# Kernel optimization log

Measured on AMD Instinct MI355X. Metric: run time of the kernel, lower is better.

## Reference

```python
import jax, jax.numpy as jnp
import numpy as np

D_MODEL = 1024
N_HEADS = 16
D_K = D_MODEL // N_HEADS


def setup_inputs() -> dict:
    key = jax.random.key(0)
    ks = jax.random.split(key, 12)
    B, S, D, H = 2, 2048, D_MODEL, N_HEADS
    s = 1.0 / np.sqrt(D)
    inp = {
        "x": jax.random.normal(ks[0], (B, S, D), jnp.float32),
        "Wq": jax.random.normal(ks[1], (D, D), jnp.float32) * s,
        "bq": jnp.zeros((D,), jnp.float32),
        "Wk": jax.random.normal(ks[2], (D, D), jnp.float32) * s,
        "bk": jnp.zeros((D,), jnp.float32),
        "Wv": jax.random.normal(ks[3], (D, D), jnp.float32) * s,
        "bv": jnp.zeros((D,), jnp.float32),
        "Wo": jax.random.normal(ks[4], (D, D), jnp.float32) * s,
        "bo": jnp.zeros((D,), jnp.float32),
        "Wp": jax.random.normal(ks[5], (D, H), jnp.float32) * s,
        "bp": jnp.zeros((H,), jnp.float32),
        "alpha": jax.random.normal(ks[6], (H,), jnp.float32) * 0.1,
    }
    return inp


def reference(x, Wq, bq, Wk, bk, Wv, bv, Wo, bo, Wp, bp, alpha):
    B, S, D = x.shape
    H, dk = N_HEADS, D_K
    scale = dk ** -0.5
    # projections -> (B, H, S, dk)
    Q = (x @ Wq + bq).reshape(B, S, H, dk).transpose(0, 2, 1, 3)
    K = (x @ Wk + bk).reshape(B, S, H, dk).transpose(0, 2, 1, 3)
    V = (x @ Wv + bv).reshape(B, S, H, dk).transpose(0, 2, 1, 3)
    scores = jnp.einsum("bhid,bhjd->bhij", Q, K) * scale  # (B,H,S,S)
    # phase derived from x: (B,S,H) -> (B,H,S)
    phase = (x @ Wp + bp).transpose(0, 2, 1)
    # coherence(i,j) = cos(phi_i - phi_j), per batch/head
    coherence = jnp.cos(phase[:, :, :, None] - phase[:, :, None, :])
    scores = scores + alpha[None, :, None, None] * coherence
    attn = jax.nn.softmax(scores, axis=-1)
    out = jnp.einsum("bhij,bhjd->bhid", attn, V)  # (B,H,S,dk)
    out = out.transpose(0, 2, 1, 3).reshape(B, S, D)
    return out @ Wo + bo
```

## Files before the change

kernel.cpp:

```cpp
#include <hip/hip_runtime.h>
#include <math.h>


#define S_LEN 2048
#define NHEADS 16

typedef __attribute__((ext_vector_type(8))) short short8;
typedef __attribute__((ext_vector_type(4))) float floatx4;
typedef __attribute__((ext_vector_type(2))) float float2v;
typedef __attribute__((ext_vector_type(4))) unsigned int uintx4;

__device__ inline unsigned short f2bf(float f) {
    union { float f; unsigned int i; } v; v.f = f;
    unsigned int u = v.i;
    return (unsigned short)((u + 0x7fffu + ((u >> 16) & 1u)) >> 16);
}
__device__ inline unsigned int pack2_bf16(float hi, float lo) {
    union { float f; unsigned int u; } a, b; a.f = hi; b.f = lo;
    return __builtin_amdgcn_perm(a.u, b.u, 0x07060302u);
}
__device__ inline void async_copy16(const unsigned short* src, unsigned short* dst_lds) {
    __builtin_amdgcn_global_load_lds(
        (const __attribute__((address_space(1))) unsigned int*)(src),
        (__attribute__((address_space(3))) unsigned int*)(dst_lds), 16, 0, 0);
}
__device__ inline void async_copy4(const float* src, float* dst_lds) {
    __builtin_amdgcn_global_load_lds(
        (const __attribute__((address_space(1))) unsigned int*)(src),
        (__attribute__((address_space(3))) unsigned int*)(dst_lds), 4, 0, 0);
}

__global__ __launch_bounds__(256) void prep_kernel(
    const float* __restrict__ x, const float* __restrict__ Wp,
    const float* __restrict__ bp,
    const float* __restrict__ w0, const float* __restrict__ w1,
    const float* __restrict__ w2, const float* __restrict__ w3,
    unsigned short* __restrict__ d0, unsigned short* __restrict__ d1,
    unsigned short* __restrict__ d2, unsigned short* __restrict__ d3,
    float* __restrict__ cosP, float* __restrict__ sinP,
    unsigned short* __restrict__ xb) {
    __shared__ __align__(16) unsigned short shmem[64 * 72];
    int t = threadIdx.x;
    if (blockIdx.x < 4096) {
        float* red = reinterpret_cast<float*>(shmem);
        int bid = blockIdx.x;
        int b = bid >> 11, s = bid & 2047;
        int h = t & 15, c = t >> 4;
        const float* xr = x + (size_t)bid * 1024;
        {
            float4 xv = *reinterpret_cast<const float4*>(&xr[t * 4]);
            uint2 o;
            o.x = (unsigned int)f2bf(xv.x) | ((unsigned int)f2bf(xv.y) << 16);
            o.y = (unsigned int)f2bf(xv.z) | ((unsigned int)f2bf(xv.w) << 16);
            *reinterpret_cast<uint2*>(&xb[(size_t)bid * 1024 + t * 4]) = o;
        }
        float acc = 0.f;
#pragma unroll 8
        for (int kk = 0; kk < 64; kk++) {
            int k = c * 64 + kk;
            acc += xr[k] * Wp[k * 16 + h];
        }
        red[t] = acc;
        __syncthreads();
        if (t < 16) {
            float sum = 0.f;
#pragma unroll
            for (int c2 = 0; c2 < 16; c2++) sum += red[c2 * 16 + t];
            sum += bp[t];
            float sv, cv;
            __sincosf(sum, &sv, &cv);
            size_t o = ((size_t)b * NHEADS + t) * S_LEN + s;
            cosP[o] = cv; sinP[o] = sv;
        }
    } else {
        unsigned short (*tile)[72] = reinterpret_cast<unsigned short (*)[72]>(shmem);
        int bid = blockIdx.x - 4096;
        int mat = bid >> 8;
        int tl  = bid & 255;
        int tr = tl >> 4, tc = tl & 15;
        const float* src    = (mat == 0) ? w0 : (mat == 1) ? w1 : (mat == 2) ? w2 : w3;
        unsigned short* dst = (mat == 0) ? d0 : (mat == 1) ? d1 : (mat == 2) ? d2 : d3;
        int col = t & 63, rbase = (t >> 6) * 16;
#pragma unroll
        for (int i = 0; i < 16; i++) {
            int row = rbase + i;
            tile[row][col] = f2bf(src[(size_t)(tr * 64 + row) * 1024 + tc * 64 + col]);
        }
        __syncthreads();
#pragma unroll
        for (int i = 0; i < 16; i++) {
            int row = rbase + i;
            dst[(size_t)(tc * 64 + row) * 1024 + tr * 64 + col] = tile[col][row];
        }
    }
}

template <int MT>
__global__ __launch_bounds__(256) void gemm_bt(
    const unsigned short* __restrict__ A, const unsigned short* __restrict__ BT,
    int N, int mode,
    const float* __restrict__ b0, const float* __restrict__ b1,
    const float* __restrict__ b2,
    unsigned short* __restrict__ o0, unsigned short* __restrict__ o1,
    unsigned short* __restrict__ o2, float* __restrict__ of) {
    __shared__ __align__(16) unsigned short As[MT * 32];
    __shared__ __align__(16) unsigned short Bs[128 * 32];
    const int K = 1024;
    const int MI = MT / 32;
    int t = threadIdx.x;
    int mBase = blockIdx.x * MT;
    int nBase = blockIdx.y * 128;
    int w = t >> 6, lane = t & 63, l15 = lane & 15, quad = lane >> 4;
    int wm = (w & 1) * (MT / 2), wn = (w >> 1) * 64;
    floatx4 acc[MI][4];
#pragma unroll
    for (int i = 0; i < MI; i++)
#pragma unroll
        for (int j = 0; j < 4; j++) acc[i][j] = (floatx4){0.f, 0.f, 0.f, 0.f};

    int arow = t >> 2, aseg = (t & 3) * 8;
    for (int k0 = 0; k0 < K; k0 += 32) {
        __syncthreads();
#pragma unroll
        for (int i = 0; i < MT / 64; i++)
            async_copy16(&A[(size_t)(mBase + i * 64 + arow) * K + k0 + aseg],
                         &As[(i * 64 + arow) * 32 + aseg]);
#pragma unroll
        for (int i = 0; i < 2; i++)
            async_copy16(&BT[(size_t)(nBase + i * 64 + arow) * K + k0 + aseg],
                         &Bs[(i * 64 + arow) * 32 + aseg]);
        __syncthreads();
        short8 af[MI], bfr[4];
#pragma unroll
        for (int mi = 0; mi < MI; mi++)
            af[mi] = *reinterpret_cast<const short8*>(&As[(wm + mi * 16 + l15) * 32 + quad * 8]);
#pragma unroll
        for (int ni = 0; ni < 4; ni++)
            bfr[ni] = *reinterpret_cast<const short8*>(&Bs[(wn + ni * 16 + l15) * 32 + quad * 8]);
#pragma unroll
        for (int mi = 0; mi < MI; mi++)
#pragma unroll
            for (int ni = 0; ni < 4; ni++)
                acc[mi][ni] = __builtin_amdgcn_mfma_f32_16x16x32_bf16(af[mi], bfr[ni], acc[mi][ni], 0, 0, 0);
    }

#pragma unroll
    for (int mi = 0; mi < MI; mi++) {
        int rowB = mBase + wm + mi * 16 + quad * 4;
#pragma unroll
        for (int ni = 0; ni < 4; ni++) {
            int col = nBase + wn + ni * 16 + l15;
            if (mode == 0) {
                float bias = b0[col];
#pragma unroll
                for (int r = 0; r < 4; r++) {
                    of[(size_t)(rowB + r) * N + col] = acc[mi][ni][r] + bias;
                }
            } else {
                int mat = col >> 10, nn = col & 1023;
                int h = nn >> 6, d = nn & 63;
                int b = rowB >> 11, sidx = rowB & 2047;
                if (mat == 2) {
                    float bv = b2[nn];
                    int jj = sidx & 63;
                    int a2 = jj >> 5, c2 = (jj >> 4) & 1, bb = jj & 15;
                    size_t rowOff = ((size_t)((b * NHEADS + h) * 64 + d)) * S_LEN +
                                    (sidx & ~63) + a2 * 32 + c2;
#pragma unroll
                    for (int r = 0; r < 4; r++)
                        o2[rowOff + 2 * (bb + r)] = f2bf(acc[mi][ni][r] + bv);
                } else {
                    const float* bias  = (mat == 0) ? b0 : b1;
                    unsigned short* op = (mat == 0) ? o0 : o1;
                    float bv = bias[nn];
                    float scl = (mat == 0) ? 0.18033688f : 1.0f;
#pragma unroll
                    for (int r = 0; r < 4; r++) {
                        float cv = (acc[mi][ni][r] + bv) * scl;
                        op[(((size_t)b * NHEADS + h) * S_LEN + (sidx + r)) * 64 + d] = f2bf(cv);
                    }
                }
            }
        }
    }
}

__global__ __launch_bounds__(1024) void attn_kernel(
    const unsigned short* __restrict__ Qg, const unsigned short* __restrict__ Kg,
    const unsigned short* __restrict__ VTg,
    const float* __restrict__ cosP, const float* __restrict__ sinP,
    const float* __restrict__ alpha, unsigned short* __restrict__ ctx) {
    __shared__ __align__(16) unsigned short KsB[2][64 * 64];
    __shared__ __align__(16) unsigned short VtB[2][64 * 64];
    __shared__ __align__(16) float csB[2][128];
    __shared__ __align__(16) unsigned short Plb[16][16 * 72];

    int x = blockIdx.x;
    int bh = (x & 7) * 4 + (x >> 6);
    int qt = (x >> 3) & 7;
    int t = threadIdx.x, w = t >> 6, lane = t & 63, l15 = lane & 15, quad = lane >> 4;
    int m0 = qt * 256 + w * 16;
    size_t base = (size_t)bh * (S_LEN * 64);
    size_t phBase = (size_t)bh * S_LEN;
    const float L2E = 1.44269504f;

    int th = t & 511;
    int sj = th >> 3, sg = th & 7;
    int srot = ((sg - (sj & 7)) & 7) * 8;
    bool stK = (t < 512);

    short8 qf[2];
#pragma unroll
    for (int c = 0; c < 2; c++)
        qf[c] = *reinterpret_cast<const short8*>(
            &Qg[base + (size_t)(m0 + l15) * 64 + c * 32 + quad * 8]);

    float alph = alpha[bh & 15] * L2E;
    float2v ci2[2], si2[2];
#pragma unroll
    for (int hh = 0; hh < 2; hh++) {
        size_t o = phBase + m0 + quad * 4 + hh * 2;
        ci2[hh] = (float2v){alph * cosP[o], alph * cosP[o + 1]};
        si2[hh] = (float2v){alph * sinP[o], alph * sinP[o + 1]};
    }

    {
        if (stK) async_copy16(&Kg[base + (size_t)sj * 64 + srot], &KsB[0][th * 8]);
        else     async_copy16(&VTg[base + (size_t)sj * S_LEN + srot], &VtB[0][th * 8]);
        if (w == 4)      async_copy4(&cosP[phBase + lane], &csB[0][lane]);
        else if (w == 5) async_copy4(&sinP[phBase + lane], &csB[0][64 + lane]);
    }

    floatx4 oacc[4], lacc;
#pragma unroll
    for (int tt = 0; tt < 4; tt++) oacc[tt] = (floatx4){0.f, 0.f, 0.f, 0.f};
    lacc = (floatx4){0.f, 0.f, 0.f, 0.f};
    const short8 ones8 = {(short)0x3F80, (short)0x3F80, (short)0x3F80, (short)0x3F80,
                          (short)0x3F80, (short)0x3F80, (short)0x3F80, (short)0x3F80};

    int rot = l15 & 7;
    int cb0 = 16 * ((quad + rot) & 7);
    int cb1 = 16 * ((quad + 4 + rot) & 7);

    for (int kt = 0; kt < 32; kt++) {
        int p = kt & 1;
        __syncthreads();
        if (kt < 31) {
            int kn = kt + 1, pn = p ^ 1;
            if (stK) async_copy16(&Kg[base + (size_t)(kn * 64 + sj) * 64 + srot], &KsB[pn][th * 8]);
            else     async_copy16(&VTg[base + (size_t)sj * S_LEN + kn * 64 + srot], &VtB[pn][th * 8]);
            if (w == 4)      async_copy4(&cosP[phBase + kn * 64 + lane], &csB[pn][lane]);
            else if (w == 5) async_copy4(&sinP[phBase + kn * 64 + lane], &csB[pn][64 + lane]);
        }

        floatx4 st[4];
#pragma unroll
        for (int jt = 0; jt < 4; jt++) {
            const char* kr = (const char*)&KsB[p][(jt * 16 + l15) * 64];
            short8 kf0 = *reinterpret_cast<const short8*>(kr + cb0);
            short8 kf1 = *reinterpret_cast<const short8*>(kr + cb1);
            floatx4 s = (floatx4){0.f, 0.f, 0.f, 0.f};
            s = __builtin_amdgcn_mfma_f32_16x16x32_bf16(qf[0], kf0, s, 0, 0, 0);
            s = __builtin_amdgcn_mfma_f32_16x16x32_bf16(qf[1], kf1, s, 0, 0, 0);
            st[jt] = s;
        }

        float cjv[4], sjv[4];
#pragma unroll
        for (int jt = 0; jt < 4; jt++) {
            cjv[jt] = csB[p][jt * 16 + l15];
            sjv[jt] = csB[p][64 + jt * 16 + l15];
        }

        unsigned int* pl = reinterpret_cast<unsigned int*>(&Plb[w][0]);
#pragma unroll
        for (int rp = 0; rp < 2; rp++) {
            float2v a0, a1, a2, a3;
            {
                float2v s0 = (float2v){st[0][rp * 2], st[0][rp * 2 + 1]};
                float2v s1 = (float2v){st[1][rp * 2], st[1][rp * 2 + 1]};
                float2v s2 = (float2v){st[2][rp * 2], st[2][rp * 2 + 1]};
                float2v s3 = (float2v){st[3][rp * 2], st[3][rp * 2 + 1]};
                a0 = si2[rp] * sjv[0] + (ci2[rp] * cjv[0] + s0);
                a1 = si2[rp] * sjv[1] + (ci2[rp] * cjv[1] + s1);
                a2 = si2[rp] * sjv[2] + (ci2[rp] * cjv[2] + s2);
                a3 = si2[rp] * sjv[3] + (ci2[rp] * cjv[3] + s3);
            }
            int row = quad * 4 + rp * 2;
            pl[row * 36 + l15]      = pack2_bf16(__builtin_amdgcn_exp2f(a1.x),
                                                 __builtin_amdgcn_exp2f(a0.x));
            pl[row * 36 + 16 + l15] = pack2_bf16(__builtin_amdgcn_exp2f(a3.x),
                                                 __builtin_amdgcn_exp2f(a2.x));
            pl[(row + 1) * 36 + l15]      = pack2_bf16(__builtin_amdgcn_exp2f(a1.y),
                                                       __builtin_amdgcn_exp2f(a0.y));
            pl[(row + 1) * 36 + 16 + l15] = pack2_bf16(__builtin_amdgcn_exp2f(a3.y),
                                                       __builtin_amdgcn_exp2f(a2.y));
        }

        short8 pf[2];
#pragma unroll
        for (int c = 0; c < 2; c++)
            pf[c] = *reinterpret_cast<const short8*>(
                &Plb[w][l15 * 72 + c * 32 + quad * 8]);

#pragma unroll
        for (int c = 0; c < 2; c++) {
            int cb = c ? cb1 : cb0;
#pragma unroll
            for (int tt = 0; tt < 4; tt++) {
                const char* vr = (const char*)&VtB[p][(tt * 16 + l15) * 64];
                short8 vf = *reinterpret_cast<const short8*>(vr + cb);
                oacc[tt] = __builtin_amdgcn_mfma_f32_16x16x32_bf16(pf[c], vf, oacc[tt], 0, 0, 0);
            }
            lacc = __builtin_amdgcn_mfma_f32_16x16x32_bf16(pf[c], ones8, lacc, 0, 0, 0);
        }
    }

    int b = bh >> 4, h = bh & 15;
    float inv[4];
#pragma unroll
    for (int r = 0; r < 4; r++) inv[r] = 1.0f / lacc[r];
#pragma unroll
    for (int tt = 0; tt < 4; tt++)
#pragma unroll
        for (int r = 0; r < 4; r++) {
            int srow = m0 + quad * 4 + r;
            ctx[((size_t)(b * S_LEN + srow)) * 1024 + h * 64 + tt * 16 + l15] =
                f2bf(oacc[tt][r] * inv[r]);
        }
}

extern "C" void kernel_launch(void* const* d_in, const int* in_sizes, int n_in,
                              void* d_out, int out_size, void* d_ws, size_t ws_size,
                              hipStream_t stream) {
    const float* x     = (const float*)d_in[0];
    const float* Wq    = (const float*)d_in[1];
    const float* bq    = (const float*)d_in[2];
    const float* Wk    = (const float*)d_in[3];
    const float* bk    = (const float*)d_in[4];
    const float* Wv    = (const float*)d_in[5];
    const float* bv    = (const float*)d_in[6];
    const float* Wo    = (const float*)d_in[7];
    const float* bo    = (const float*)d_in[8];
    const float* Wp    = (const float*)d_in[9];
    const float* bp    = (const float*)d_in[10];
    const float* alpha = (const float*)d_in[11];
    float* out = (float*)d_out;

    const size_t MB = 1048576;
    char* ws = (char*)d_ws;
    unsigned short* WT   = (unsigned short*)(ws);
    unsigned short* WoT  = (unsigned short*)(ws + 6 * MB);
    unsigned short* xb   = (unsigned short*)(ws + 8 * MB);
    unsigned short* ctx  = (unsigned short*)(ws + 8 * MB);
    unsigned short* Qw   = (unsigned short*)(ws + 16 * MB);
    unsigned short* Kw   = (unsigned short*)(ws + 24 * MB);
    unsigned short* VTg  = (unsigned short*)(ws + 32 * MB);
    float* cosP          = (float*)(ws + 40 * MB);
    float* sinP          = (float*)(ws + 40 * MB + 262144);

    prep_kernel<<<dim3(5120), dim3(256), 0, stream>>>(
        x, Wp, bp, Wq, Wk, Wv, Wo,
        WT, WT + 1048576, WT + 2097152, WoT, cosP, sinP, xb);
    gemm_bt<128><<<dim3(32, 24), dim3(256), 0, stream>>>(
        xb, WT, 3072, 1, bq, bk, bv, Qw, Kw, VTg, (float*)nullptr);
    attn_kernel<<<dim3(256), dim3(1024), 0, stream>>>(
        Qw, Kw, VTg, cosP, sinP, alpha, ctx);
    gemm_bt<64><<<dim3(64, 8), dim3(256), 0, stream>>>(
        ctx, WoT, 1024, 0, bo, bo, bo,
        (unsigned short*)nullptr, (unsigned short*)nullptr,
        (unsigned short*)nullptr, out);
}
```

Before: 215.2 us.

## Give each attention wave two 16-row query tiles with half the threads per block

The attention kernel now launches 512 threads per block instead of 1024, and each wave handles 32 query rows as two 16-row sub-tiles. K/V fragments loaded from LDS are reused across both sub-tiles, which halves LDS reads per score and PV MFMA. Each thread now issues both the K and the V async copy. The change doubles accumulator and Q register state per wave, which raises register pressure, and it halves the waves per block available to hide latency.

```diff
diff --git a/kernel.cpp b/kernel.cpp
--- a/kernel.cpp
+++ b/kernel.cpp
@@ -185,7 +185,7 @@
     }
 }
 
-__global__ __launch_bounds__(1024) void attn_kernel(
+__global__ __launch_bounds__(512, 4) void attn_kernel(
     const unsigned short* __restrict__ Qg, const unsigned short* __restrict__ Kg,
     const unsigned short* __restrict__ VTg,
     const float* __restrict__ cosP, const float* __restrict__ sinP,
@@ -193,48 +193,53 @@
     __shared__ __align__(16) unsigned short KsB[2][64 * 64];
     __shared__ __align__(16) unsigned short VtB[2][64 * 64];
     __shared__ __align__(16) float csB[2][128];
-    __shared__ __align__(16) unsigned short Plb[16][16 * 72];
+    __shared__ __align__(16) unsigned short Plb[8][32 * 72];
 
     int x = blockIdx.x;
     int bh = (x & 7) * 4 + (x >> 6);
     int qt = (x >> 3) & 7;
     int t = threadIdx.x, w = t >> 6, lane = t & 63, l15 = lane & 15, quad = lane >> 4;
-    int m0 = qt * 256 + w * 16;
+    int m0 = qt * 256 + w * 32;
     size_t base = (size_t)bh * (S_LEN * 64);
     size_t phBase = (size_t)bh * S_LEN;
     const float L2E = 1.44269504f;
 
-    int th = t & 511;
-    int sj = th >> 3, sg = th & 7;
+    int sj = t >> 3, sg = t & 7;
     int srot = ((sg - (sj & 7)) & 7) * 8;
-    bool stK = (t < 512);
-
-    short8 qf[2];
-#pragma unroll
-    for (int c = 0; c < 2; c++)
-        qf[c] = *reinterpret_cast<const short8*>(
-            &Qg[base + (size_t)(m0 + l15) * 64 + c * 32 + quad * 8]);
+
+    short8 qf[2][2];
+#pragma unroll
+    for (int rh = 0; rh < 2; rh++)
+#pragma unroll
+        for (int c = 0; c < 2; c++)
+            qf[rh][c] = *reinterpret_cast<const short8*>(
+                &Qg[base + (size_t)(m0 + rh * 16 + l15) * 64 + c * 32 + quad * 8]);
 
     float alph = alpha[bh & 15] * L2E;
-    float2v ci2[2], si2[2];
-#pragma unroll
-    for (int hh = 0; hh < 2; hh++) {
-        size_t o = phBase + m0 + quad * 4 + hh * 2;
-        ci2[hh] = (float2v){alph * cosP[o], alph * cosP[o + 1]};
-        si2[hh] = (float2v){alph * sinP[o], alph * sinP[o + 1]};
-    }
+    float2v ci2[2][2], si2[2][2];
+#pragma unroll
+    for (int rh = 0; rh < 2; rh++)
+#pragma unroll
+        for (int hh = 0; hh < 2; hh++) {
+            size_t o = phBase + m0 + rh * 16 + quad * 4 + hh * 2;
+            ci2[rh][hh] = (float2v){alph * cosP[o], alph * cosP[o + 1]};
+            si2[rh][hh] = (float2v){alph * sinP[o], alph * sinP[o + 1]};
+        }
 
     {
-        if (stK) async_copy16(&Kg[base + (size_t)sj * 64 + srot], &KsB[0][th * 8]);
-        else     async_copy16(&VTg[base + (size_t)sj * S_LEN + srot], &VtB[0][th * 8]);
-        if (w == 4)      async_copy4(&cosP[phBase + lane], &csB[0][lane]);
-        else if (w == 5) async_copy4(&sinP[phBase + lane], &csB[0][64 + lane]);
-    }
-
-    floatx4 oacc[4], lacc;
-#pragma unroll
-    for (int tt = 0; tt < 4; tt++) oacc[tt] = (floatx4){0.f, 0.f, 0.f, 0.f};
-    lacc = (floatx4){0.f, 0.f, 0.f, 0.f};
+        async_copy16(&Kg[base + (size_t)sj * 64 + srot], &KsB[0][t * 8]);
+        async_copy16(&VTg[base + (size_t)sj * S_LEN + srot], &VtB[0][t * 8]);
+        if (w == 2)      async_copy4(&cosP[phBase + lane], &csB[0][lane]);
+        else if (w == 3) async_copy4(&sinP[phBase + lane], &csB[0][64 + lane]);
+    }
+
+    floatx4 oacc[2][4], lacc[2];
+#pragma unroll
+    for (int rh = 0; rh < 2; rh++) {
+#pragma unroll
+        for (int tt = 0; tt < 4; tt++) oacc[rh][tt] = (floatx4){0.f, 0.f, 0.f, 0.f};
+        lacc[rh] = (floatx4){0.f, 0.f, 0.f, 0.f};
+    }
     const short8 ones8 = {(short)0x3F80, (short)0x3F80, (short)0x3F80, (short)0x3F80,
                           (short)0x3F80, (short)0x3F80, (short)0x3F80, (short)0x3F80};
 
@@ -247,22 +252,25 @@
         __syncthreads();
         if (kt < 31) {
             int kn = kt + 1, pn = p ^ 1;
-            if (stK) async_copy16(&Kg[base + (size_t)(kn * 64 + sj) * 64 + srot], &KsB[pn][th * 8]);
-            else     async_copy16(&VTg[base + (size_t)sj * S_LEN + kn * 64 + srot], &VtB[pn][th * 8]);
-            if (w == 4)      async_copy4(&cosP[phBase + kn * 64 + lane], &csB[pn][lane]);
-            else if (w == 5) async_copy4(&sinP[phBase + kn * 64 + lane], &csB[pn][64 + lane]);
-        }
-
-        floatx4 st[4];
+            async_copy16(&Kg[base + (size_t)(kn * 64 + sj) * 64 + srot], &KsB[pn][t * 8]);
+            async_copy16(&VTg[base + (size_t)sj * S_LEN + kn * 64 + srot], &VtB[pn][t * 8]);
+            if (w == 2)      async_copy4(&cosP[phBase + kn * 64 + lane], &csB[pn][lane]);
+            else if (w == 3) async_copy4(&sinP[phBase + kn * 64 + lane], &csB[pn][64 + lane]);
+        }
+
+        floatx4 st[2][4];
 #pragma unroll
         for (int jt = 0; jt < 4; jt++) {
             const char* kr = (const char*)&KsB[p][(jt * 16 + l15) * 64];
             short8 kf0 = *reinterpret_cast<const short8*>(kr + cb0);
             short8 kf1 = *reinterpret_cast<const short8*>(kr + cb1);
-            floatx4 s = (floatx4){0.f, 0.f, 0.f, 0.f};
-            s = __builtin_amdgcn_mfma_f32_16x16x32_bf16(qf[0], kf0, s, 0, 0, 0);
-            s = __builtin_amdgcn_mfma_f32_16x16x32_bf16(qf[1], kf1, s, 0, 0, 0);
-            st[jt] = s;
+#pragma unroll
+            for (int rh = 0; rh < 2; rh++) {
+                floatx4 s = (floatx4){0.f, 0.f, 0.f, 0.f};
+                s = __builtin_amdgcn_mfma_f32_16x16x32_bf16(qf[rh][0], kf0, s, 0, 0, 0);
+                s = __builtin_amdgcn_mfma_f32_16x16x32_bf16(qf[rh][1], kf1, s, 0, 0, 0);
+                st[rh][jt] = s;
+            }
         }
 
         float cjv[4], sjv[4];
@@ -274,34 +282,38 @@
 
         unsigned int* pl = reinterpret_cast<unsigned int*>(&Plb[w][0]);
 #pragma unroll
-        for (int rp = 0; rp < 2; rp++) {
-            float2v a0, a1, a2, a3;
-            {
-                float2v s0 = (float2v){st[0][rp * 2], st[0][rp * 2 + 1]};
-                float2v s1 = (float2v){st[1][rp * 2], st[1][rp * 2 + 1]};
-                float2v s2 = (float2v){st[2][rp * 2], st[2][rp * 2 + 1]};
-                float2v s3 = (float2v){st[3][rp * 2], st[3][rp * 2 + 1]};
-                a0 = si2[rp] * sjv[0] + (ci2[rp] * cjv[0] + s0);
-                a1 = si2[rp] * sjv[1] + (ci2[rp] * cjv[1] + s1);
-                a2 = si2[rp] * sjv[2] + (ci2[rp] * cjv[2] + s2);
-                a3 = si2[rp] * sjv[3] + (ci2[rp] * cjv[3] + s3);
-            }
-            int row = quad * 4 + rp * 2;
-            pl[row * 36 + l15]      = pack2_bf16(__builtin_amdgcn_exp2f(a1.x),
-                                                 __builtin_amdgcn_exp2f(a0.x));
-            pl[row * 36 + 16 + l15] = pack2_bf16(__builtin_amdgcn_exp2f(a3.x),
-                                                 __builtin_amdgcn_exp2f(a2.x));
-            pl[(row + 1) * 36 + l15]      = pack2_bf16(__builtin_amdgcn_exp2f(a1.y),
-                                                       __builtin_amdgcn_exp2f(a0.y));
-            pl[(row + 1) * 36 + 16 + l15] = pack2_bf16(__builtin_amdgcn_exp2f(a3.y),
-                                                       __builtin_amdgcn_exp2f(a2.y));
-        }
-
-        short8 pf[2];
-#pragma unroll
-        for (int c = 0; c < 2; c++)
-            pf[c] = *reinterpret_cast<const short8*>(
-                &Plb[w][l15 * 72 + c * 32 + quad * 8]);
+        for (int rh = 0; rh < 2; rh++)
+#pragma unroll
+            for (int rp = 0; rp < 2; rp++) {
+                float2v a0, a1, a2, a3;
+                {
+                    float2v s0 = (float2v){st[rh][0][rp * 2], st[rh][0][rp * 2 + 1]};
+                    float2v s1 = (float2v){st[rh][1][rp * 2], st[rh][1][rp * 2 + 1]};
+                    float2v s2 = (float2v){st[rh][2][rp * 2], st[rh][2][rp * 2 + 1]};
+                    float2v s3 = (float2v){st[rh][3][rp * 2], st[rh][3][rp * 2 + 1]};
+                    a0 = si2[rh][rp] * sjv[0] + (ci2[rh][rp] * cjv[0] + s0);
+                    a1 = si2[rh][rp] * sjv[1] + (ci2[rh][rp] * cjv[1] + s1);
+                    a2 = si2[rh][rp] * sjv[2] + (ci2[rh][rp] * cjv[2] + s2);
+                    a3 = si2[rh][rp] * sjv[3] + (ci2[rh][rp] * cjv[3] + s3);
+                }
+                int row = rh * 16 + quad * 4 + rp * 2;
+                pl[row * 36 + l15]      = pack2_bf16(__builtin_amdgcn_exp2f(a1.x),
+                                                     __builtin_amdgcn_exp2f(a0.x));
+                pl[row * 36 + 16 + l15] = pack2_bf16(__builtin_amdgcn_exp2f(a3.x),
+                                                     __builtin_amdgcn_exp2f(a2.x));
+                pl[(row + 1) * 36 + l15]      = pack2_bf16(__builtin_amdgcn_exp2f(a1.y),
+                                                           __builtin_amdgcn_exp2f(a0.y));
+                pl[(row + 1) * 36 + 16 + l15] = pack2_bf16(__builtin_amdgcn_exp2f(a3.y),
+                                                           __builtin_amdgcn_exp2f(a2.y));
+            }
+
+        short8 pf[2][2];
+#pragma unroll
+        for (int rh = 0; rh < 2; rh++)
+#pragma unroll
+            for (int c = 0; c < 2; c++)
+                pf[rh][c] = *reinterpret_cast<const short8*>(
+                    &Plb[w][(rh * 16 + l15) * 72 + c * 32 + quad * 8]);
 
 #pragma unroll
         for (int c = 0; c < 2; c++) {
@@ -310,24 +322,29 @@
             for (int tt = 0; tt < 4; tt++) {
                 const char* vr = (const char*)&VtB[p][(tt * 16 + l15) * 64];
                 short8 vf = *reinterpret_cast<const short8*>(vr + cb);
-                oacc[tt] = __builtin_amdgcn_mfma_f32_16x16x32_bf16(pf[c], vf, oacc[tt], 0, 0, 0);
-            }
-            lacc = __builtin_amdgcn_mfma_f32_16x16x32_bf16(pf[c], ones8, lacc, 0, 0, 0);
+                oacc[0][tt] = __builtin_amdgcn_mfma_f32_16x16x32_bf16(pf[0][c], vf, oacc[0][tt], 0, 0, 0);
+                oacc[1][tt] = __builtin_amdgcn_mfma_f32_16x16x32_bf16(pf[1][c], vf, oacc[1][tt], 0, 0, 0);
+            }
+            lacc[0] = __builtin_amdgcn_mfma_f32_16x16x32_bf16(pf[0][c], ones8, lacc[0], 0, 0, 0);
+            lacc[1] = __builtin_amdgcn_mfma_f32_16x16x32_bf16(pf[1][c], ones8, lacc[1], 0, 0, 0);
         }
     }
 
     int b = bh >> 4, h = bh & 15;
-    float inv[4];
-#pragma unroll
-    for (int r = 0; r < 4; r++) inv[r] = 1.0f / lacc[r];
-#pragma unroll
-    for (int tt = 0; tt < 4; tt++)
-#pragma unroll
-        for (int r = 0; r < 4; r++) {
-            int srow = m0 + quad * 4 + r;
-            ctx[((size_t)(b * S_LEN + srow)) * 1024 + h * 64 + tt * 16 + l15] =
-                f2bf(oacc[tt][r] * inv[r]);
-        }
+#pragma unroll
+    for (int rh = 0; rh < 2; rh++) {
+        float inv[4];
+#pragma unroll
+        for (int r = 0; r < 4; r++) inv[r] = 1.0f / lacc[rh][r];
+#pragma unroll
+        for (int tt = 0; tt < 4; tt++)
+#pragma unroll
+            for (int r = 0; r < 4; r++) {
+                int srow = m0 + rh * 16 + quad * 4 + r;
+                ctx[((size_t)(b * S_LEN + srow)) * 1024 + h * 64 + tt * 16 + l15] =
+                    f2bf(oacc[rh][tt][r] * inv[r]);
+            }
+    }
 }
 
 extern "C" void kernel_launch(void* const* d_in, const int* in_sizes, int n_in,
@@ -364,7 +381,7 @@
         WT, WT + 1048576, WT + 2097152, WoT, cosP, sinP, xb);
     gemm_bt<128><<<dim3(32, 24), dim3(256), 0, stream>>>(
         xb, WT, 3072, 1, bq, bk, bv, Qw, Kw, VTg, (float*)nullptr);
-    attn_kernel<<<dim3(256), dim3(1024), 0, stream>>>(
+    attn_kernel<<<dim3(256), dim3(512), 0, stream>>>(
         Qw, Kw, VTg, cosP, sinP, alpha, ctx);
     gemm_bt<64><<<dim3(64, 8), dim3(256), 0, stream>>>(
         ctx, WoT, 1024, 0, bo, bo, bo,
```

Measured after the change: 260.0 us. 20.8% more time.
